# Kernel tuning notes

Measured on AMD Instinct MI355X. Metric: run time of the kernel, lower is better.

## Reference

```python
import jax, jax.numpy as jnp
import numpy as np

N = 50000
E = 800000
NEG_SLOPE = 0.2  # PyG GATConv default negative_slope


def _gat_layer(x, src, dst, W, a_src, a_dst, b, concat):
    # x: [N, Fin]; src/dst: [Etot] (self-loops already appended)
    H, O = a_src.shape
    n = x.shape[0]
    h = (x @ W).reshape(n, H, O)                      # [N, H, O]
    e_src = jnp.einsum('nho,ho->nh', h, a_src)        # [N, H]
    e_dst = jnp.einsum('nho,ho->nh', h, a_dst)
    alpha = e_src[src] + e_dst[dst]                   # [Etot, H]
    alpha = jnp.where(alpha >= 0, alpha, NEG_SLOPE * alpha)
    # segment softmax over destination nodes
    amax = jax.ops.segment_max(alpha, dst, num_segments=n)
    ex = jnp.exp(alpha - amax[dst])
    denom = jax.ops.segment_sum(ex, dst, num_segments=n)
    att = ex / (denom[dst] + 1e-16)                   # [Etot, H]
    msg = h[src] * att[:, :, None]                    # [Etot, H, O]
    agg = jax.ops.segment_sum(msg, dst, num_segments=n)  # [N, H, O]
    out = agg.reshape(n, H * O) if concat else agg.mean(axis=1)
    return out + b


def setup_inputs() -> dict:
    key = jax.random.key(0)
    k0, k1 = jax.random.split(key)
    inp = {
        'x': jax.random.normal(k0, (N, 2), jnp.float32),
        'edge_index': jax.random.randint(k1, (2, E), 0, N),
    }
    s = 0.1
    dims = [(2, 4, 64), (256, 4, 64), (256, 1, 2)]
    for i, (fin, H, O) in enumerate(dims):
        kw, ks, kd = jax.random.split(jax.random.fold_in(key, i + 10), 3)
        inp[f'W{i}'] = jax.random.normal(kw, (fin, H * O), jnp.float32) * s
        inp[f'a_src{i}'] = jax.random.normal(ks, (H, O), jnp.float32) * s
        inp[f'a_dst{i}'] = jax.random.normal(kd, (H, O), jnp.float32) * s
        inp[f'b{i}'] = jnp.zeros((H * O if i < 2 else O,), jnp.float32)
    return inp


def reference(x, edge_index, W0, a_src0, a_dst0, b0, W1, a_src1, a_dst1, b1,
              W2, a_src2, a_dst2, b2):
    n = x.shape[0]
    loops = jnp.arange(n, dtype=edge_index.dtype)  # PyG add_self_loops=True
    src = jnp.concatenate([edge_index[0], loops])
    dst = jnp.concatenate([edge_index[1], loops])
    h = jax.nn.relu(_gat_layer(x, src, dst, W0, a_src0, a_dst0, b0, True))
    h = jax.nn.relu(_gat_layer(h, src, dst, W1, a_src1, a_dst1, b1, True))
    h = jax.nn.relu(_gat_layer(h, src, dst, W2, a_src2, a_dst2, b2, False))
    return h
```

## Files before the change

kernel.cpp:

```cpp
#include <hip/hip_runtime.h>
#include <math.h>


typedef __attribute__((ext_vector_type(8))) short s16x8;
typedef __attribute__((ext_vector_type(4))) float f32x4;
typedef unsigned short u16;

__device__ __forceinline__ float wred_sum(float v){
  #pragma unroll
  for (int m = 32; m > 0; m >>= 1) v += __shfl_xor(v, m, 64);
  return v;
}
__device__ __forceinline__ void wred_sum4(float4& v){
  #pragma unroll
  for (int m = 32; m > 0; m >>= 1){
    v.x += __shfl_xor(v.x, m, 64);
    v.y += __shfl_xor(v.y, m, 64);
    v.z += __shfl_xor(v.z, m, 64);
    v.w += __shfl_xor(v.w, m, 64);
  }
}
__device__ __forceinline__ u16 bf16_rne(float x){
  unsigned int u = __float_as_uint(x);
  unsigned int r = u + 0x7FFFu + ((u >> 16) & 1u);
  return (u16)(r >> 16);
}

__global__ __launch_bounds__(256) void k_setup(const float* __restrict__ W1, u16* __restrict__ WhT,
                                               u16* __restrict__ WlT,
                                               const float* __restrict__ W0, const float* __restrict__ as0,
                                               const float* __restrict__ ad0, float* __restrict__ vs,
                                               int* __restrict__ deg, int N, int nblk_deg){
  int b = blockIdx.x;
  if (b < nblk_deg){
    int i = b * 256 + threadIdx.x;
    if (i < N) deg[i] = 1;
  } else if (b < nblk_deg + 256){
    int k = b - nblk_deg, j = threadIdx.x;
    float w = W1[k * 256 + j];
    u16 h = bf16_rne(w);
    float hf = __uint_as_float(((unsigned int)h) << 16);
    WhT[j * 256 + k] = h;
    WlT[j * 256 + k] = bf16_rne(w - hf);
  } else {
    int t = threadIdx.x;
    if (t < 8){
      int j = t >> 2, h = t & 3;
      float ss = 0.f, dd = 0.f;
      #pragma unroll 8
      for (int o = 0; o < 64; o++){
        float w = W0[j * 256 + h * 64 + o];
        ss = fmaf(w, as0[h * 64 + o], ss);
        dd = fmaf(w, ad0[h * 64 + o], dd);
      }
      vs[j * 4 + h]     = ss;
      vs[8 + j * 4 + h] = dd;
    }
  }
}

__global__ __launch_bounds__(256) void k_hist(const int* __restrict__ dst, int E, int* deg){
  int e = blockIdx.x * 256 + threadIdx.x;
  if (e < E) atomicAdd(&deg[dst[e]], 1);
}

__global__ __launch_bounds__(256) void k_scan_local(const int* __restrict__ deg, int* __restrict__ rowptr,
                                                    int* __restrict__ bsum, int N){
  __shared__ int sb[256];
  int t = threadIdx.x;
  int base = blockIdx.x * 2048 + t * 8;
  int d[8], s = 0;
  #pragma unroll
  for (int k = 0; k < 8; k++){
    d[k] = (base + k < N) ? deg[base + k] : 0;
    s += d[k];
  }
  sb[t] = s;
  __syncthreads();
  for (int off = 1; off < 256; off <<= 1){
    int v = (t >= off) ? sb[t - off] : 0;
    __syncthreads();
    sb[t] += v;
    __syncthreads();
  }
  int run = (t == 0) ? 0 : sb[t - 1];
  #pragma unroll
  for (int k = 0; k < 8; k++){
    if (base + k < N) rowptr[base + k] = run;
    run += d[k];
  }
  if (t == 255) bsum[blockIdx.x] = sb[255];
}

__global__ __launch_bounds__(256) void k_finish(int* __restrict__ rowptr, const int* __restrict__ bsum,
                                                int* __restrict__ ssrc, int* __restrict__ cursor,
                                                int N, int nb){
  __shared__ int off_sh;
  int i = blockIdx.x * 256 + threadIdx.x;
  if (threadIdx.x == 0){
    int bk = blockIdx.x >> 3;
    int s = 0;
    for (int k = 0; k < bk; k++) s += bsum[k];
    off_sh = s;
  }
  __syncthreads();
  if (i < N){
    int p = rowptr[i] + off_sh;
    rowptr[i] = p;
    ssrc[p] = i;
    cursor[i] = p + 1;
  }
  if (i == 0){
    int s = 0;
    for (int k = 0; k < nb; k++) s += bsum[k];
    rowptr[N] = s;
  }
}

__global__ __launch_bounds__(256) void k_scatter(const int* __restrict__ src, const int* __restrict__ dst,
                                                 int E, int* cursor, int* ssrc){
  int e = blockIdx.x * 256 + threadIdx.x;
  if (e < E){ int p = atomicAdd(&cursor[dst[e]], 1); ssrc[p] = src[e]; }
}

__global__ __launch_bounds__(256) void k_edge0(const float* __restrict__ X, const float* __restrict__ vs,
                                               const int* __restrict__ rowptr, const int* __restrict__ ssrc,
                                               float* __restrict__ agg2, int N){
  int lane = threadIdx.x & 63;
  int n = blockIdx.x * 4 + (threadIdx.x >> 6);
  if (n >= N) return;
  int start = rowptr[n], deg = rowptr[n + 1] - start;
  float4 va = ((const float4*)vs)[0], vb = ((const float4*)vs)[1];
  float4 vc = ((const float4*)vs)[2], vd = ((const float4*)vs)[3];
  float2 xn = ((const float2*)X)[n];
  float4 ed4;
  ed4.x = fmaf(xn.x, vc.x, xn.y * vd.x); ed4.y = fmaf(xn.x, vc.y, xn.y * vd.y);
  ed4.z = fmaf(xn.x, vc.z, xn.y * vd.z); ed4.w = fmaf(xn.x, vc.w, xn.y * vd.w);

  float4 den = make_float4(0.f,0.f,0.f,0.f);
  float4 a0  = make_float4(0.f,0.f,0.f,0.f);
  float4 a1  = make_float4(0.f,0.f,0.f,0.f);
  for (int i = lane; i < deg; i += 64){
    int s = ssrc[start + i];
    float2 xs = ((const float2*)X)[s];
    float4 e;
    e.x = fmaf(xs.x, va.x, fmaf(xs.y, vb.x, ed4.x));
    e.y = fmaf(xs.x, va.y, fmaf(xs.y, vb.y, ed4.y));
    e.z = fmaf(xs.x, va.z, fmaf(xs.y, vb.z, ed4.z));
    e.w = fmaf(xs.x, va.w, fmaf(xs.y, vb.w, ed4.w));
    e.x = fmaxf(e.x, 0.2f*e.x); e.y = fmaxf(e.y, 0.2f*e.y);
    e.z = fmaxf(e.z, 0.2f*e.z); e.w = fmaxf(e.w, 0.2f*e.w);
    float4 wt;
    wt.x = __expf(e.x); wt.y = __expf(e.y);
    wt.z = __expf(e.z); wt.w = __expf(e.w);
    den.x += wt.x; den.y += wt.y; den.z += wt.z; den.w += wt.w;
    a0.x = fmaf(wt.x, xs.x, a0.x); a0.y = fmaf(wt.y, xs.x, a0.y);
    a0.z = fmaf(wt.z, xs.x, a0.z); a0.w = fmaf(wt.w, xs.x, a0.w);
    a1.x = fmaf(wt.x, xs.y, a1.x); a1.y = fmaf(wt.y, xs.y, a1.y);
    a1.z = fmaf(wt.z, xs.y, a1.z); a1.w = fmaf(wt.w, xs.y, a1.w);
  }
  wred_sum4(den); wred_sum4(a0); wred_sum4(a1);

  if (lane == 0){
    float4 inv;
    inv.x = 1.f / (den.x + 1e-16f); inv.y = 1.f / (den.y + 1e-16f);
    inv.z = 1.f / (den.z + 1e-16f); inv.w = 1.f / (den.w + 1e-16f);
    float4 gA, gB;
    gA.x = a0.x * inv.x; gA.y = a1.x * inv.x;
    gA.z = a0.y * inv.y; gA.w = a1.y * inv.y;
    gB.x = a0.z * inv.z; gB.y = a1.z * inv.z;
    gB.z = a0.w * inv.w; gB.w = a1.w * inv.w;
    float4* g = (float4*)(agg2 + (size_t)n * 8);
    g[0] = gA; g[1] = gB;
  }
}

__global__ __launch_bounds__(256) void k_l1_mfma(const float* __restrict__ agg2,
                                                 const float* __restrict__ W0, const float* __restrict__ b0,
                                                 const u16* __restrict__ WhT, const u16* __restrict__ WlT,
                                                 const float* __restrict__ as_, const float* __restrict__ ad_,
                                                 u16* __restrict__ Hh16, float* __restrict__ ES,
                                                 float* __restrict__ ED, int N){
  __shared__ u16 Ah[64 * 32], Al[64 * 32];
  __shared__ u16 Bh[256 * 32], Bl[256 * 32];
  int t = threadIdx.x;
  int wv = t >> 6, lane = t & 63;
  int lr = lane & 15, lg = lane >> 4;
  int rb = blockIdx.x * 64;

  f32x4 acc[16];
  #pragma unroll
  for (int c = 0; c < 16; c++) acc[c] = (f32x4){0.f, 0.f, 0.f, 0.f};

  int arow = t >> 2, aseg = t & 3;
  int agrow = rb + arow;
  float4 ga = make_float4(0.f,0.f,0.f,0.f), gb = make_float4(0.f,0.f,0.f,0.f);
  if (agrow < N){
    const float4* g = (const float4*)(agg2 + (size_t)agrow * 8);
    ga = g[0]; gb = g[1];
  }

  for (int ks = 0; ks < 8; ks++){
    int k0 = ks * 32;
    __syncthreads();
    {
      int c0 = k0 + aseg * 8;
      int h = c0 >> 6;
      float g0 = (h==0)?ga.x:(h==1)?ga.z:(h==2)?gb.x:gb.z;
      float g1 = (h==0)?ga.y:(h==1)?ga.w:(h==2)?gb.y:gb.w;
      float4 w0a = *(const float4*)(W0 + c0);
      float4 w0b = *(const float4*)(W0 + c0 + 4);
      float4 w1a = *(const float4*)(W0 + 256 + c0);
      float4 w1b = *(const float4*)(W0 + 256 + c0 + 4);
      float4 bba = *(const float4*)(b0 + c0);
      float4 bbb = *(const float4*)(b0 + c0 + 4);
      float xv[8];
      xv[0] = fmaxf(fmaf(g0, w0a.x, fmaf(g1, w1a.x, bba.x)), 0.f);
      xv[1] = fmaxf(fmaf(g0, w0a.y, fmaf(g1, w1a.y, bba.y)), 0.f);
      xv[2] = fmaxf(fmaf(g0, w0a.z, fmaf(g1, w1a.z, bba.z)), 0.f);
      xv[3] = fmaxf(fmaf(g0, w0a.w, fmaf(g1, w1a.w, bba.w)), 0.f);
      xv[4] = fmaxf(fmaf(g0, w0b.x, fmaf(g1, w1b.x, bbb.x)), 0.f);
      xv[5] = fmaxf(fmaf(g0, w0b.y, fmaf(g1, w1b.y, bbb.y)), 0.f);
      xv[6] = fmaxf(fmaf(g0, w0b.z, fmaf(g1, w1b.z, bbb.z)), 0.f);
      xv[7] = fmaxf(fmaf(g0, w0b.w, fmaf(g1, w1b.w, bbb.w)), 0.f);
      if (agrow >= N){
        #pragma unroll
        for (int i = 0; i < 8; i++) xv[i] = 0.f;
      }
      union { u16 us[8]; uint4 v; } ph, pl;
      #pragma unroll
      for (int i = 0; i < 8; i++){
        u16 h16 = bf16_rne(xv[i]);
        float hf = __uint_as_float(((unsigned int)h16) << 16);
        ph.us[i] = h16;
        pl.us[i] = bf16_rne(xv[i] - hf);
      }
      *(uint4*)&Ah[arow * 32 + aseg * 8] = ph.v;
      *(uint4*)&Al[arow * 32 + aseg * 8] = pl.v;
    }
    #pragma unroll
    for (int i = 0; i < 4; i++){
      int chunk = i * 256 + t;
      int j = chunk >> 2, seg = chunk & 3;
      *(uint4*)&Bh[j * 32 + seg * 8] = *(const uint4*)&WhT[j * 256 + k0 + seg * 8];
      *(uint4*)&Bl[j * 32 + seg * 8] = *(const uint4*)&WlT[j * 256 + k0 + seg * 8];
    }
    __syncthreads();
    s16x8 ah = *(const s16x8*)&Ah[(wv * 16 + lr) * 32 + lg * 8];
    s16x8 al = *(const s16x8*)&Al[(wv * 16 + lr) * 32 + lg * 8];
    #pragma unroll
    for (int c = 0; c < 16; c++){
      s16x8 bh = *(const s16x8*)&Bh[(c * 16 + lr) * 32 + lg * 8];
      s16x8 bl = *(const s16x8*)&Bl[(c * 16 + lr) * 32 + lg * 8];
      acc[c] = __builtin_amdgcn_mfma_f32_16x16x32_bf16(ah, bh, acc[c], 0, 0, 0);
      acc[c] = __builtin_amdgcn_mfma_f32_16x16x32_bf16(ah, bl, acc[c], 0, 0, 0);
      acc[c] = __builtin_amdgcn_mfma_f32_16x16x32_bf16(al, bh, acc[c], 0, 0, 0);
    }
  }

  #pragma unroll
  for (int q = 0; q < 4; q++){
    int n = rb + wv * 16 + lg * 4 + q;
    if (n < N){
      union { _Float16 h[16]; uint4 v[2]; } pk;
      #pragma unroll
      for (int c = 0; c < 16; c++) pk.h[c] = (_Float16)acc[c][q];
      uint4* dstp = (uint4*)(Hh16 + (size_t)n * 256 + lr * 16);
      dstp[0] = pk.v[0];
      dstp[1] = pk.v[1];
    }
  }
  float es_p[4][4], ed_p[4][4];
  #pragma unroll
  for (int h = 0; h < 4; h++)
    #pragma unroll
    for (int q = 0; q < 4; q++){ es_p[h][q] = 0.f; ed_p[h][q] = 0.f; }
  #pragma unroll
  for (int c = 0; c < 16; c++){
    float asv = as_[c * 16 + lr];
    float adv = ad_[c * 16 + lr];
    int h = c >> 2;
    #pragma unroll
    for (int q = 0; q < 4; q++){
      es_p[h][q] = fmaf(acc[c][q], asv, es_p[h][q]);
      ed_p[h][q] = fmaf(acc[c][q], adv, ed_p[h][q]);
    }
  }
  #pragma unroll
  for (int h = 0; h < 4; h++)
    #pragma unroll
    for (int q = 0; q < 4; q++){
      #pragma unroll
      for (int mk = 1; mk < 16; mk <<= 1){
        es_p[h][q] += __shfl_xor(es_p[h][q], mk, 64);
        ed_p[h][q] += __shfl_xor(ed_p[h][q], mk, 64);
      }
    }
  if (lr == 0){
    #pragma unroll
    for (int q = 0; q < 4; q++){
      int n = rb + wv * 16 + lg * 4 + q;
      if (n < N){
        #pragma unroll
        for (int h = 0; h < 4; h++){
          ES[n * 4 + h] = es_p[h][q];
          ED[n * 4 + h] = ed_p[h][q];
        }
      }
    }
  }
}

__device__ __forceinline__ void agg_rows16(const u16* __restrict__ Hh, const int* ssh, const float* wrow,
                                           int cl, int lane, float* acc){
  union Cv { uint2 u; _Float16 h[4]; };
  int j = 0;
  for (; j + 7 < cl; j += 8){
    Cv r0, r1, r2, r3, r4, r5, r6, r7;
    float w0=wrow[j],w1=wrow[j+1],w2=wrow[j+2],w3=wrow[j+3];
    float w4=wrow[j+4],w5=wrow[j+5],w6=wrow[j+6],w7=wrow[j+7];
    r0.u = *(const uint2*)(Hh + (size_t)ssh[j  ] * 256 + 4*lane);
    r1.u = *(const uint2*)(Hh + (size_t)ssh[j+1] * 256 + 4*lane);
    r2.u = *(const uint2*)(Hh + (size_t)ssh[j+2] * 256 + 4*lane);
    r3.u = *(const uint2*)(Hh + (size_t)ssh[j+3] * 256 + 4*lane);
    r4.u = *(const uint2*)(Hh + (size_t)ssh[j+4] * 256 + 4*lane);
    r5.u = *(const uint2*)(Hh + (size_t)ssh[j+5] * 256 + 4*lane);
    r6.u = *(const uint2*)(Hh + (size_t)ssh[j+6] * 256 + 4*lane);
    r7.u = *(const uint2*)(Hh + (size_t)ssh[j+7] * 256 + 4*lane);
    #pragma unroll
    for (int k = 0; k < 4; k++) acc[k] = fmaf(w0, (float)r0.h[k], acc[k]);
    #pragma unroll
    for (int k = 0; k < 4; k++) acc[k] = fmaf(w1, (float)r1.h[k], acc[k]);
    #pragma unroll
    for (int k = 0; k < 4; k++) acc[k] = fmaf(w2, (float)r2.h[k], acc[k]);
    #pragma unroll
    for (int k = 0; k < 4; k++) acc[k] = fmaf(w3, (float)r3.h[k], acc[k]);
    #pragma unroll
    for (int k = 0; k < 4; k++) acc[k] = fmaf(w4, (float)r4.h[k], acc[k]);
    #pragma unroll
    for (int k = 0; k < 4; k++) acc[k] = fmaf(w5, (float)r5.h[k], acc[k]);
    #pragma unroll
    for (int k = 0; k < 4; k++) acc[k] = fmaf(w6, (float)r6.h[k], acc[k]);
    #pragma unroll
    for (int k = 0; k < 4; k++) acc[k] = fmaf(w7, (float)r7.h[k], acc[k]);
  }
  for (; j + 3 < cl; j += 4){
    Cv r0, r1, r2, r3;
    float w0=wrow[j],w1=wrow[j+1],w2=wrow[j+2],w3=wrow[j+3];
    r0.u = *(const uint2*)(Hh + (size_t)ssh[j  ] * 256 + 4*lane);
    r1.u = *(const uint2*)(Hh + (size_t)ssh[j+1] * 256 + 4*lane);
    r2.u = *(const uint2*)(Hh + (size_t)ssh[j+2] * 256 + 4*lane);
    r3.u = *(const uint2*)(Hh + (size_t)ssh[j+3] * 256 + 4*lane);
    #pragma unroll
    for (int k = 0; k < 4; k++) acc[k] = fmaf(w0, (float)r0.h[k], acc[k]);
    #pragma unroll
    for (int k = 0; k < 4; k++) acc[k] = fmaf(w1, (float)r1.h[k], acc[k]);
    #pragma unroll
    for (int k = 0; k < 4; k++) acc[k] = fmaf(w2, (float)r2.h[k], acc[k]);
    #pragma unroll
    for (int k = 0; k < 4; k++) acc[k] = fmaf(w3, (float)r3.h[k], acc[k]);
  }
  for (; j < cl; ++j){
    Cv r0;
    float w0 = wrow[j];
    r0.u = *(const uint2*)(Hh + (size_t)ssh[j] * 256 + 4*lane);
    #pragma unroll
    for (int k = 0; k < 4; k++) acc[k] = fmaf(w0, (float)r0.h[k], acc[k]);
  }
}

__global__ __launch_bounds__(64) void k_edge1(const u16* __restrict__ Hh16, const float* __restrict__ ES,
                                              const float* __restrict__ ED, const int* __restrict__ rowptr,
                                              const int* __restrict__ ssrc, const float* __restrict__ b1,
                                              const float* __restrict__ W2,
                                              const float* __restrict__ as2, const float* __restrict__ ad2,
                                              float* __restrict__ P2, int N){
  __shared__ int   ssh[64];
  __shared__ float wsh[4][68];
  int lane = threadIdx.x;
  int n = blockIdx.x;
  int myhead = lane & 3;
  int start = rowptr[n], deg = rowptr[n + 1] - start;
  float4 ed4 = ((const float4*)ED)[n];

  float accv[4] = {0.f, 0.f, 0.f, 0.f};
  float4 den = make_float4(0.f,0.f,0.f,0.f);

  for (int base = 0; base < deg; base += 64){
    int i = base + lane;
    float4 wt = make_float4(0.f,0.f,0.f,0.f);
    int s = 0;
    if (i < deg){
      s = ssrc[start + i];
      float4 e = ((const float4*)ES)[s];
      e.x += ed4.x; e.y += ed4.y; e.z += ed4.z; e.w += ed4.w;
      e.x = fmaxf(e.x, 0.2f*e.x); e.y = fmaxf(e.y, 0.2f*e.y);
      e.z = fmaxf(e.z, 0.2f*e.z); e.w = fmaxf(e.w, 0.2f*e.w);
      wt.x = __expf(e.x); wt.y = __expf(e.y);
      wt.z = __expf(e.z); wt.w = __expf(e.w);
    }
    den.x += wt.x; den.y += wt.y; den.z += wt.z; den.w += wt.w;
    ssh[lane] = s;
    wsh[0][lane] = wt.x; wsh[1][lane] = wt.y;
    wsh[2][lane] = wt.z; wsh[3][lane] = wt.w;
    __syncthreads();
    agg_rows16(Hh16, ssh, wsh[myhead], min(deg - base, 64), lane, accv);
    __syncthreads();
  }

  wred_sum4(den);
  float d = (myhead==0)?den.x:(myhead==1)?den.y:(myhead==2)?den.z:den.w;
  float inv = 1.f / (d + 1e-16f);
  int c0 = 64 * (lane & 3) + (lane >> 2);
  float p0 = 0.f, p1 = 0.f;
  #pragma unroll
  for (int j = 0; j < 4; j++){
    int col = c0 + 16 * j;
    float v = fmaxf(fmaf(accv[j], inv, b1[col]), 0.f);
    float2 w2 = ((const float2*)W2)[col];
    p0 = fmaf(v, w2.x, p0);
    p1 = fmaf(v, w2.y, p1);
  }
  p0 = wred_sum(p0); p1 = wred_sum(p1);
  if (lane == 0){
    float4 o;
    o.x = p0; o.y = p1;
    o.z = p0*as2[0] + p1*as2[1];
    o.w = p0*ad2[0] + p1*ad2[1];
    ((float4*)P2)[n] = o;
  }
}

__global__ __launch_bounds__(256) void k_edge2(const float* __restrict__ P2, const int* __restrict__ rowptr,
                                               const int* __restrict__ ssrc, const float* __restrict__ bias,
                                               float* __restrict__ Out, int N){
  int lane = threadIdx.x & 63;
  int n = blockIdx.x * 4 + (threadIdx.x >> 6);
  if (n >= N) return;
  int start = rowptr[n], deg = rowptr[n + 1] - start;
  float edn = ((const float4*)P2)[n].w;
  float den = 0.f, a0 = 0.f, a1 = 0.f;
  for (int i = lane; i < deg; i += 64){
    int s = ssrc[start + i];
    float4 p = ((const float4*)P2)[s];
    float a = p.z + edn; a = fmaxf(a, 0.2f * a);
    float w = __expf(a);
    den += w;
    a0 = fmaf(w, p.x, a0);
    a1 = fmaf(w, p.y, a1);
  }
  den = wred_sum(den); a0 = wred_sum(a0); a1 = wred_sum(a1);
  if (lane == 0){
    float inv = 1.f / (den + 1e-16f);
    Out[n*2]     = fmaxf(a0 * inv + bias[0], 0.f);
    Out[n*2 + 1] = fmaxf(a1 * inv + bias[1], 0.f);
  }
}

extern "C" void kernel_launch(void* const* d_in, const int* in_sizes, int n_in,
                              void* d_out, int out_size, void* d_ws, size_t ws_size,
                              hipStream_t stream) {
  const float* x   = (const float*)d_in[0];
  const int*   ei  = (const int*)  d_in[1];
  const float* W0  = (const float*)d_in[2];
  const float* as0 = (const float*)d_in[3];
  const float* ad0 = (const float*)d_in[4];
  const float* b0  = (const float*)d_in[5];
  const float* W1  = (const float*)d_in[6];
  const float* as1 = (const float*)d_in[7];
  const float* ad1 = (const float*)d_in[8];
  const float* b1  = (const float*)d_in[9];
  const float* W2  = (const float*)d_in[10];
  const float* as2 = (const float*)d_in[11];
  const float* ad2 = (const float*)d_in[12];
  const float* b2  = (const float*)d_in[13];

  int N = in_sizes[0] / 2;
  int E = in_sizes[1] / 2;
  const int* src = ei;
  const int* dst = ei + E;

  char* ws = (char*)d_ws;
  size_t off = 0;
  auto alc = [&](size_t bytes){ size_t o = off; off += (bytes + 255) & ~(size_t)255; return o; };
  int*   deg    = (int*)(ws + alc((size_t)N * 4));
  int*   rowptr = (int*)(ws + alc((size_t)(N + 1) * 4));
  int*   cursor = (int*)(ws + alc((size_t)N * 4));
  int*   ssrc   = (int*)(ws + alc((size_t)(E + N) * 4));
  u16*   Hh16   = (u16*)  (ws + alc((size_t)N * 256 * 2));
  float* agg2   = (float*)(ws + alc((size_t)N * 8 * 4));
  float* es1    = (float*)(ws + alc((size_t)N * 4 * 4));
  float* ed1    = (float*)(ws + alc((size_t)N * 4 * 4));
  float* P2     = (float*)(ws + alc((size_t)N * 4 * 4));
  u16*   wht    = (u16*)  (ws + alc((size_t)256 * 256 * 2));
  u16*   wlt    = (u16*)  (ws + alc((size_t)256 * 256 * 2));
  float* vs     = (float*)(ws + alc(16 * 4));
  int*   bsum   = (int*)(ws + alc(64 * 4));
  float* out    = (float*)d_out;

  int nblk_deg = (N + 255) / 256;
  int nb = (N + 2047) / 2048;

  k_setup     <<<nblk_deg + 257, 256, 0, stream>>>(W1, wht, wlt, W0, as0, ad0, vs, deg, N, nblk_deg);
  k_hist      <<<(E + 255)/256, 256, 0, stream>>>(dst, E, deg);
  k_scan_local<<<nb, 256, 0, stream>>>(deg, rowptr, bsum, N);
  k_finish    <<<nblk_deg, 256, 0, stream>>>(rowptr, bsum, ssrc, cursor, N, nb);
  k_scatter   <<<(E + 255)/256, 256, 0, stream>>>(src, dst, E, cursor, ssrc);

  k_edge0  <<<(N + 3)/4, 256, 0, stream>>>(x, vs, rowptr, ssrc, agg2, N);
  k_l1_mfma<<<(N + 63)/64, 256, 0, stream>>>(agg2, W0, b0, wht, wlt, as1, ad1, Hh16, es1, ed1, N);
  k_edge1  <<<N, 64, 0, stream>>>(Hh16, es1, ed1, rowptr, ssrc, b1, W2, as2, ad2, P2, N);
  k_edge2  <<<(N + 3)/4, 256, 0, stream>>>(P2, rowptr, ssrc, b2, out, N);
}
```

Before: 345.0 us.

## Fuse layer-0 edge aggregation into layer-1 MFMA kernel and merge histogram into setup

Computes the layer-0 attention aggregation inside the layer-1 GEMM kernel, now 512 threads with 128 rows per block, and hands results to the A-tile producers through a lane-select. This removes the agg2 round trip and one launch. The degree histogram moves into the setup kernel, with deg zeroed by a memset and the self-loop +1 added in the scan, which drops another launch. In exchange, each wave serially processes 16 nodes before any MFMA work starts, and the larger block may lower occupancy.

```diff
diff --git a/kernel.cpp b/kernel.cpp
--- a/kernel.cpp
+++ b/kernel.cpp
@@ -26,17 +26,18 @@
   return (u16)(r >> 16);
 }
 
-__global__ __launch_bounds__(256) void k_setup(const float* __restrict__ W1, u16* __restrict__ WhT,
-                                               u16* __restrict__ WlT,
-                                               const float* __restrict__ W0, const float* __restrict__ as0,
-                                               const float* __restrict__ ad0, float* __restrict__ vs,
-                                               int* __restrict__ deg, int N, int nblk_deg){
+__global__ __launch_bounds__(256) void k_prep(const int* __restrict__ dst, int E, int* __restrict__ deg,
+                                              const float* __restrict__ W1, u16* __restrict__ WhT,
+                                              u16* __restrict__ WlT,
+                                              const float* __restrict__ W0, const float* __restrict__ as0,
+                                              const float* __restrict__ ad0, float* __restrict__ vs,
+                                              int nhist){
   int b = blockIdx.x;
-  if (b < nblk_deg){
-    int i = b * 256 + threadIdx.x;
-    if (i < N) deg[i] = 1;
-  } else if (b < nblk_deg + 256){
-    int k = b - nblk_deg, j = threadIdx.x;
+  if (b < nhist){
+    int e = b * 256 + threadIdx.x;
+    if (e < E) atomicAdd(&deg[dst[e]], 1);
+  } else if (b < nhist + 256){
+    int k = b - nhist, j = threadIdx.x;
     float w = W1[k * 256 + j];
     u16 h = bf16_rne(w);
     float hf = __uint_as_float(((unsigned int)h) << 16);
@@ -59,11 +60,6 @@
   }
 }
 
-__global__ __launch_bounds__(256) void k_hist(const int* __restrict__ dst, int E, int* deg){
-  int e = blockIdx.x * 256 + threadIdx.x;
-  if (e < E) atomicAdd(&deg[dst[e]], 1);
-}
-
 __global__ __launch_bounds__(256) void k_scan_local(const int* __restrict__ deg, int* __restrict__ rowptr,
                                                     int* __restrict__ bsum, int N){
   __shared__ int sb[256];
@@ -72,7 +68,7 @@
   int d[8], s = 0;
   #pragma unroll
   for (int k = 0; k < 8; k++){
-    d[k] = (base + k < N) ? deg[base + k] : 0;
+    d[k] = (base + k < N) ? (deg[base + k] + 1) : 0;
     s += d[k];
   }
   sb[t] = s;
@@ -123,45 +119,54 @@
   if (e < E){ int p = atomicAdd(&cursor[dst[e]], 1); ssrc[p] = src[e]; }
 }
 
-__global__ __launch_bounds__(256) void k_edge0(const float* __restrict__ X, const float* __restrict__ vs,
-                                               const int* __restrict__ rowptr, const int* __restrict__ ssrc,
-                                               float* __restrict__ agg2, int N){
-  int lane = threadIdx.x & 63;
-  int n = blockIdx.x * 4 + (threadIdx.x >> 6);
-  if (n >= N) return;
-  int start = rowptr[n], deg = rowptr[n + 1] - start;
+__global__ __launch_bounds__(512) void k_l1f(const float* __restrict__ X, const float* __restrict__ vs,
+                                             const int* __restrict__ rowptr, const int* __restrict__ ssrc,
+                                             const float* __restrict__ W0, const float* __restrict__ b0,
+                                             const u16* __restrict__ WhT, const u16* __restrict__ WlT,
+                                             const float* __restrict__ as_, const float* __restrict__ ad_,
+                                             u16* __restrict__ Hh16, float* __restrict__ ES,
+                                             float* __restrict__ ED, int N){
+  __shared__ u16 Ah[128 * 32], Al[128 * 32];
+  __shared__ u16 Bh[256 * 32], Bl[256 * 32];
+  int t = threadIdx.x;
+  int wv = t >> 6, lane = t & 63;
+  int lr = lane & 15, lg = lane >> 4;
+  int rb = blockIdx.x * 128;
+
   float4 va = ((const float4*)vs)[0], vb = ((const float4*)vs)[1];
   float4 vc = ((const float4*)vs)[2], vd = ((const float4*)vs)[3];
-  float2 xn = ((const float2*)X)[n];
-  float4 ed4;
-  ed4.x = fmaf(xn.x, vc.x, xn.y * vd.x); ed4.y = fmaf(xn.x, vc.y, xn.y * vd.y);
-  ed4.z = fmaf(xn.x, vc.z, xn.y * vd.z); ed4.w = fmaf(xn.x, vc.w, xn.y * vd.w);
-
-  float4 den = make_float4(0.f,0.f,0.f,0.f);
-  float4 a0  = make_float4(0.f,0.f,0.f,0.f);
-  float4 a1  = make_float4(0.f,0.f,0.f,0.f);
-  for (int i = lane; i < deg; i += 64){
-    int s = ssrc[start + i];
-    float2 xs = ((const float2*)X)[s];
-    float4 e;
-    e.x = fmaf(xs.x, va.x, fmaf(xs.y, vb.x, ed4.x));
-    e.y = fmaf(xs.x, va.y, fmaf(xs.y, vb.y, ed4.y));
-    e.z = fmaf(xs.x, va.z, fmaf(xs.y, vb.z, ed4.z));
-    e.w = fmaf(xs.x, va.w, fmaf(xs.y, vb.w, ed4.w));
-    e.x = fmaxf(e.x, 0.2f*e.x); e.y = fmaxf(e.y, 0.2f*e.y);
-    e.z = fmaxf(e.z, 0.2f*e.z); e.w = fmaxf(e.w, 0.2f*e.w);
-    float4 wt;
-    wt.x = __expf(e.x); wt.y = __expf(e.y);
-    wt.z = __expf(e.z); wt.w = __expf(e.w);
-    den.x += wt.x; den.y += wt.y; den.z += wt.z; den.w += wt.w;
-    a0.x = fmaf(wt.x, xs.x, a0.x); a0.y = fmaf(wt.y, xs.x, a0.y);
-    a0.z = fmaf(wt.z, xs.x, a0.z); a0.w = fmaf(wt.w, xs.x, a0.w);
-    a1.x = fmaf(wt.x, xs.y, a1.x); a1.y = fmaf(wt.y, xs.y, a1.y);
-    a1.z = fmaf(wt.z, xs.y, a1.z); a1.w = fmaf(wt.w, xs.y, a1.w);
-  }
-  wred_sum4(den); wred_sum4(a0); wred_sum4(a1);
-
-  if (lane == 0){
+  float4 myga = make_float4(0.f,0.f,0.f,0.f), mygb = make_float4(0.f,0.f,0.f,0.f);
+  for (int i = 0; i < 16; i++){
+    int n = rb + wv * 16 + i;
+    if (n >= N) break;
+    int start = rowptr[n], deg = rowptr[n + 1] - start;
+    float2 xn = ((const float2*)X)[n];
+    float4 ed4;
+    ed4.x = fmaf(xn.x, vc.x, xn.y * vd.x); ed4.y = fmaf(xn.x, vc.y, xn.y * vd.y);
+    ed4.z = fmaf(xn.x, vc.z, xn.y * vd.z); ed4.w = fmaf(xn.x, vc.w, xn.y * vd.w);
+    float4 den = make_float4(0.f,0.f,0.f,0.f);
+    float4 a0  = make_float4(0.f,0.f,0.f,0.f);
+    float4 a1  = make_float4(0.f,0.f,0.f,0.f);
+    for (int idx = lane; idx < deg; idx += 64){
+      int s = ssrc[start + idx];
+      float2 xs = ((const float2*)X)[s];
+      float4 e;
+      e.x = fmaf(xs.x, va.x, fmaf(xs.y, vb.x, ed4.x));
+      e.y = fmaf(xs.x, va.y, fmaf(xs.y, vb.y, ed4.y));
+      e.z = fmaf(xs.x, va.z, fmaf(xs.y, vb.z, ed4.z));
+      e.w = fmaf(xs.x, va.w, fmaf(xs.y, vb.w, ed4.w));
+      e.x = fmaxf(e.x, 0.2f*e.x); e.y = fmaxf(e.y, 0.2f*e.y);
+      e.z = fmaxf(e.z, 0.2f*e.z); e.w = fmaxf(e.w, 0.2f*e.w);
+      float4 wt;
+      wt.x = __expf(e.x); wt.y = __expf(e.y);
+      wt.z = __expf(e.z); wt.w = __expf(e.w);
+      den.x += wt.x; den.y += wt.y; den.z += wt.z; den.w += wt.w;
+      a0.x = fmaf(wt.x, xs.x, a0.x); a0.y = fmaf(wt.y, xs.x, a0.y);
+      a0.z = fmaf(wt.z, xs.x, a0.z); a0.w = fmaf(wt.w, xs.x, a0.w);
+      a1.x = fmaf(wt.x, xs.y, a1.x); a1.y = fmaf(wt.y, xs.y, a1.y);
+      a1.z = fmaf(wt.z, xs.y, a1.z); a1.w = fmaf(wt.w, xs.y, a1.w);
+    }
+    wred_sum4(den); wred_sum4(a0); wred_sum4(a1);
     float4 inv;
     inv.x = 1.f / (den.x + 1e-16f); inv.y = 1.f / (den.y + 1e-16f);
     inv.z = 1.f / (den.z + 1e-16f); inv.w = 1.f / (den.w + 1e-16f);
@@ -170,23 +175,8 @@
     gA.z = a0.y * inv.y; gA.w = a1.y * inv.y;
     gB.x = a0.z * inv.z; gB.y = a1.z * inv.z;
     gB.z = a0.w * inv.w; gB.w = a1.w * inv.w;
-    float4* g = (float4*)(agg2 + (size_t)n * 8);
-    g[0] = gA; g[1] = gB;
-  }
-}
-
-__global__ __launch_bounds__(256) void k_l1_mfma(const float* __restrict__ agg2,
-                                                 const float* __restrict__ W0, const float* __restrict__ b0,
-                                                 const u16* __restrict__ WhT, const u16* __restrict__ WlT,
-                                                 const float* __restrict__ as_, const float* __restrict__ ad_,
-                                                 u16* __restrict__ Hh16, float* __restrict__ ES,
-                                                 float* __restrict__ ED, int N){
-  __shared__ u16 Ah[64 * 32], Al[64 * 32];
-  __shared__ u16 Bh[256 * 32], Bl[256 * 32];
-  int t = threadIdx.x;
-  int wv = t >> 6, lane = t & 63;
-  int lr = lane & 15, lg = lane >> 4;
-  int rb = blockIdx.x * 64;
+    if ((lane >> 2) == i){ myga = gA; mygb = gB; }
+  }
 
   f32x4 acc[16];
   #pragma unroll
@@ -194,11 +184,6 @@
 
   int arow = t >> 2, aseg = t & 3;
   int agrow = rb + arow;
-  float4 ga = make_float4(0.f,0.f,0.f,0.f), gb = make_float4(0.f,0.f,0.f,0.f);
-  if (agrow < N){
-    const float4* g = (const float4*)(agg2 + (size_t)agrow * 8);
-    ga = g[0]; gb = g[1];
-  }
 
   for (int ks = 0; ks < 8; ks++){
     int k0 = ks * 32;
@@ -206,8 +191,8 @@
     {
       int c0 = k0 + aseg * 8;
       int h = c0 >> 6;
-      float g0 = (h==0)?ga.x:(h==1)?ga.z:(h==2)?gb.x:gb.z;
-      float g1 = (h==0)?ga.y:(h==1)?ga.w:(h==2)?gb.y:gb.w;
+      float g0 = (h==0)?myga.x:(h==1)?myga.z:(h==2)?mygb.x:mygb.z;
+      float g1 = (h==0)?myga.y:(h==1)?myga.w:(h==2)?mygb.y:mygb.w;
       float4 w0a = *(const float4*)(W0 + c0);
       float4 w0b = *(const float4*)(W0 + c0 + 4);
       float4 w1a = *(const float4*)(W0 + 256 + c0);
@@ -239,8 +224,8 @@
       *(uint4*)&Al[arow * 32 + aseg * 8] = pl.v;
     }
     #pragma unroll
-    for (int i = 0; i < 4; i++){
-      int chunk = i * 256 + t;
+    for (int i = 0; i < 2; i++){
+      int chunk = i * 512 + t;
       int j = chunk >> 2, seg = chunk & 3;
       *(uint4*)&Bh[j * 32 + seg * 8] = *(const uint4*)&WhT[j * 256 + k0 + seg * 8];
       *(uint4*)&Bl[j * 32 + seg * 8] = *(const uint4*)&WlT[j * 256 + k0 + seg * 8];
@@ -488,7 +473,6 @@
   int*   cursor = (int*)(ws + alc((size_t)N * 4));
   int*   ssrc   = (int*)(ws + alc((size_t)(E + N) * 4));
   u16*   Hh16   = (u16*)  (ws + alc((size_t)N * 256 * 2));
-  float* agg2   = (float*)(ws + alc((size_t)N * 8 * 4));
   float* es1    = (float*)(ws + alc((size_t)N * 4 * 4));
   float* ed1    = (float*)(ws + alc((size_t)N * 4 * 4));
   float* P2     = (float*)(ws + alc((size_t)N * 4 * 4));
@@ -498,17 +482,18 @@
   int*   bsum   = (int*)(ws + alc(64 * 4));
   float* out    = (float*)d_out;
 
-  int nblk_deg = (N + 255) / 256;
-  int nb = (N + 2047) / 2048;
-
-  k_setup     <<<nblk_deg + 257, 256, 0, stream>>>(W1, wht, wlt, W0, as0, ad0, vs, deg, N, nblk_deg);
-  k_hist      <<<(E + 255)/256, 256, 0, stream>>>(dst, E, deg);
+  int nhist  = (E + 255) / 256;
+  int nblk_n = (N + 255) / 256;
+  int nb     = (N + 2047) / 2048;
+
+  hipMemsetAsync(deg, 0, (size_t)N * 4, stream);
+  k_prep      <<<nhist + 257, 256, 0, stream>>>(dst, E, deg, W1, wht, wlt, W0, as0, ad0, vs, nhist);
   k_scan_local<<<nb, 256, 0, stream>>>(deg, rowptr, bsum, N);
-  k_finish    <<<nblk_deg, 256, 0, stream>>>(rowptr, bsum, ssrc, cursor, N, nb);
-  k_scatter   <<<(E + 255)/256, 256, 0, stream>>>(src, dst, E, cursor, ssrc);
-
-  k_edge0  <<<(N + 3)/4, 256, 0, stream>>>(x, vs, rowptr, ssrc, agg2, N);
-  k_l1_mfma<<<(N + 63)/64, 256, 0, stream>>>(agg2, W0, b0, wht, wlt, as1, ad1, Hh16, es1, ed1, N);
-  k_edge1  <<<N, 64, 0, stream>>>(Hh16, es1, ed1, rowptr, ssrc, b1, W2, as2, ad2, P2, N);
-  k_edge2  <<<(N + 3)/4, 256, 0, stream>>>(P2, rowptr, ssrc, b2, out, N);
-}
+  k_finish    <<<nblk_n, 256, 0, stream>>>(rowptr, bsum, ssrc, cursor, N, nb);
+  k_scatter   <<<nhist, 256, 0, stream>>>(src, dst, E, cursor, ssrc);
+
+  k_l1f  <<<(N + 127)/128, 512, 0, stream>>>(x, vs, rowptr, ssrc, W0, b0, wht, wlt,
+                                             as1, ad1, Hh16, es1, ed1, N);
+  k_edge1<<<N, 64, 0, stream>>>(Hh16, es1, ed1, rowptr, ssrc, b1, W2, as2, ad2, P2, N);
+  k_edge2<<<(N + 3)/4, 256, 0, stream>>>(P2, rowptr, ssrc, b2, out, N);
+}
```

New measurement: 350.1 us. Within noise of the previous version (+1.5%).

## Widen edge1 gathers to 16-byte loads across half-waves; merge histogram into prep

Applied to the files above, without the earlier changes.

In the layer-2 aggregation kernel, each lane now loads 8 fp16 values (16 bytes) per neighbor row. The two half-waves take alternating edges, and their partial sums are combined with a cross-half shuffle before the epilogue. This halves the number of gather instructions and issues wider memory transactions per neighbor. The degree histogram is folded into the setup kernel, which removes one launch. The degree init is replaced by a memset, with the self-loop +1 moved into the scan. The epilogue column mapping and per-head normalization are rewritten to match the new accumulator layout, which risks indexing mistakes.

```diff
diff --git a/kernel.cpp b/kernel.cpp
--- a/kernel.cpp
+++ b/kernel.cpp
@@ -26,17 +26,18 @@
   return (u16)(r >> 16);
 }
 
-__global__ __launch_bounds__(256) void k_setup(const float* __restrict__ W1, u16* __restrict__ WhT,
-                                               u16* __restrict__ WlT,
-                                               const float* __restrict__ W0, const float* __restrict__ as0,
-                                               const float* __restrict__ ad0, float* __restrict__ vs,
-                                               int* __restrict__ deg, int N, int nblk_deg){
+__global__ __launch_bounds__(256) void k_prep(const int* __restrict__ dst, int E, int* __restrict__ deg,
+                                              const float* __restrict__ W1, u16* __restrict__ WhT,
+                                              u16* __restrict__ WlT,
+                                              const float* __restrict__ W0, const float* __restrict__ as0,
+                                              const float* __restrict__ ad0, float* __restrict__ vs,
+                                              int nhist){
   int b = blockIdx.x;
-  if (b < nblk_deg){
-    int i = b * 256 + threadIdx.x;
-    if (i < N) deg[i] = 1;
-  } else if (b < nblk_deg + 256){
-    int k = b - nblk_deg, j = threadIdx.x;
+  if (b < nhist){
+    int e = b * 256 + threadIdx.x;
+    if (e < E) atomicAdd(&deg[dst[e]], 1);
+  } else if (b < nhist + 256){
+    int k = b - nhist, j = threadIdx.x;
     float w = W1[k * 256 + j];
     u16 h = bf16_rne(w);
     float hf = __uint_as_float(((unsigned int)h) << 16);
@@ -59,11 +60,6 @@
   }
 }
 
-__global__ __launch_bounds__(256) void k_hist(const int* __restrict__ dst, int E, int* deg){
-  int e = blockIdx.x * 256 + threadIdx.x;
-  if (e < E) atomicAdd(&deg[dst[e]], 1);
-}
-
 __global__ __launch_bounds__(256) void k_scan_local(const int* __restrict__ deg, int* __restrict__ rowptr,
                                                     int* __restrict__ bsum, int N){
   __shared__ int sb[256];
@@ -72,7 +68,7 @@
   int d[8], s = 0;
   #pragma unroll
   for (int k = 0; k < 8; k++){
-    d[k] = (base + k < N) ? deg[base + k] : 0;
+    d[k] = (base + k < N) ? (deg[base + k] + 1) : 0;
     s += d[k];
   }
   sb[t] = s;
@@ -311,64 +307,6 @@
   }
 }
 
-__device__ __forceinline__ void agg_rows16(const u16* __restrict__ Hh, const int* ssh, const float* wrow,
-                                           int cl, int lane, float* acc){
-  union Cv { uint2 u; _Float16 h[4]; };
-  int j = 0;
-  for (; j + 7 < cl; j += 8){
-    Cv r0, r1, r2, r3, r4, r5, r6, r7;
-    float w0=wrow[j],w1=wrow[j+1],w2=wrow[j+2],w3=wrow[j+3];
-    float w4=wrow[j+4],w5=wrow[j+5],w6=wrow[j+6],w7=wrow[j+7];
-    r0.u = *(const uint2*)(Hh + (size_t)ssh[j  ] * 256 + 4*lane);
-    r1.u = *(const uint2*)(Hh + (size_t)ssh[j+1] * 256 + 4*lane);
-    r2.u = *(const uint2*)(Hh + (size_t)ssh[j+2] * 256 + 4*lane);
-    r3.u = *(const uint2*)(Hh + (size_t)ssh[j+3] * 256 + 4*lane);
-    r4.u = *(const uint2*)(Hh + (size_t)ssh[j+4] * 256 + 4*lane);
-    r5.u = *(const uint2*)(Hh + (size_t)ssh[j+5] * 256 + 4*lane);
-    r6.u = *(const uint2*)(Hh + (size_t)ssh[j+6] * 256 + 4*lane);
-    r7.u = *(const uint2*)(Hh + (size_t)ssh[j+7] * 256 + 4*lane);
-    #pragma unroll
-    for (int k = 0; k < 4; k++) acc[k] = fmaf(w0, (float)r0.h[k], acc[k]);
-    #pragma unroll
-    for (int k = 0; k < 4; k++) acc[k] = fmaf(w1, (float)r1.h[k], acc[k]);
-    #pragma unroll
-    for (int k = 0; k < 4; k++) acc[k] = fmaf(w2, (float)r2.h[k], acc[k]);
-    #pragma unroll
-    for (int k = 0; k < 4; k++) acc[k] = fmaf(w3, (float)r3.h[k], acc[k]);
-    #pragma unroll
-    for (int k = 0; k < 4; k++) acc[k] = fmaf(w4, (float)r4.h[k], acc[k]);
-    #pragma unroll
-    for (int k = 0; k < 4; k++) acc[k] = fmaf(w5, (float)r5.h[k], acc[k]);
-    #pragma unroll
-    for (int k = 0; k < 4; k++) acc[k] = fmaf(w6, (float)r6.h[k], acc[k]);
-    #pragma unroll
-    for (int k = 0; k < 4; k++) acc[k] = fmaf(w7, (float)r7.h[k], acc[k]);
-  }
-  for (; j + 3 < cl; j += 4){
-    Cv r0, r1, r2, r3;
-    float w0=wrow[j],w1=wrow[j+1],w2=wrow[j+2],w3=wrow[j+3];
-    r0.u = *(const uint2*)(Hh + (size_t)ssh[j  ] * 256 + 4*lane);
-    r1.u = *(const uint2*)(Hh + (size_t)ssh[j+1] * 256 + 4*lane);
-    r2.u = *(const uint2*)(Hh + (size_t)ssh[j+2] * 256 + 4*lane);
-    r3.u = *(const uint2*)(Hh + (size_t)ssh[j+3] * 256 + 4*lane);
-    #pragma unroll
-    for (int k = 0; k < 4; k++) acc[k] = fmaf(w0, (float)r0.h[k], acc[k]);
-    #pragma unroll
-    for (int k = 0; k < 4; k++) acc[k] = fmaf(w1, (float)r1.h[k], acc[k]);
-    #pragma unroll
-    for (int k = 0; k < 4; k++) acc[k] = fmaf(w2, (float)r2.h[k], acc[k]);
-    #pragma unroll
-    for (int k = 0; k < 4; k++) acc[k] = fmaf(w3, (float)r3.h[k], acc[k]);
-  }
-  for (; j < cl; ++j){
-    Cv r0;
-    float w0 = wrow[j];
-    r0.u = *(const uint2*)(Hh + (size_t)ssh[j] * 256 + 4*lane);
-    #pragma unroll
-    for (int k = 0; k < 4; k++) acc[k] = fmaf(w0, (float)r0.h[k], acc[k]);
-  }
-}
-
 __global__ __launch_bounds__(64) void k_edge1(const u16* __restrict__ Hh16, const float* __restrict__ ES,
                                               const float* __restrict__ ED, const int* __restrict__ rowptr,
                                               const int* __restrict__ ssrc, const float* __restrict__ b1,
@@ -379,12 +317,18 @@
   __shared__ float wsh[4][68];
   int lane = threadIdx.x;
   int n = blockIdx.x;
-  int myhead = lane & 3;
   int start = rowptr[n], deg = rowptr[n + 1] - start;
   float4 ed4 = ((const float4*)ED)[n];
 
-  float accv[4] = {0.f, 0.f, 0.f, 0.f};
+  int half = lane >> 5;
+  int l32  = lane & 31;
+  int hA = 2 * (l32 & 1);
+  int hB = hA + 1;
+  const u16* rowbase = Hh16 + 8 * l32;
+
+  float acc8[8] = {0.f,0.f,0.f,0.f,0.f,0.f,0.f,0.f};
   float4 den = make_float4(0.f,0.f,0.f,0.f);
+  union Cv { uint4 v; _Float16 h[8]; };
 
   for (int base = 0; base < deg; base += 64){
     int i = base + lane;
@@ -404,22 +348,90 @@
     wsh[0][lane] = wt.x; wsh[1][lane] = wt.y;
     wsh[2][lane] = wt.z; wsh[3][lane] = wt.w;
     __syncthreads();
-    agg_rows16(Hh16, ssh, wsh[myhead], min(deg - base, 64), lane, accv);
+    int cl = min(deg - base, 64);
+    const float* wrA = wsh[hA];
+    const float* wrB = wsh[hB];
+    int j = half;
+    for (; j + 14 < cl; j += 16){
+      int s0=ssh[j],s1=ssh[j+2],s2=ssh[j+4],s3=ssh[j+6];
+      int s4=ssh[j+8],s5=ssh[j+10],s6=ssh[j+12],s7=ssh[j+14];
+      float wa0=wrA[j],wb0=wrB[j],wa1=wrA[j+2],wb1=wrB[j+2];
+      float wa2=wrA[j+4],wb2=wrB[j+4],wa3=wrA[j+6],wb3=wrB[j+6];
+      float wa4=wrA[j+8],wb4=wrB[j+8],wa5=wrA[j+10],wb5=wrB[j+10];
+      float wa6=wrA[j+12],wb6=wrB[j+12],wa7=wrA[j+14],wb7=wrB[j+14];
+      Cv r0,r1,r2,r3,r4,r5,r6,r7;
+      r0.v = *(const uint4*)(rowbase + (size_t)s0*256);
+      r1.v = *(const uint4*)(rowbase + (size_t)s1*256);
+      r2.v = *(const uint4*)(rowbase + (size_t)s2*256);
+      r3.v = *(const uint4*)(rowbase + (size_t)s3*256);
+      r4.v = *(const uint4*)(rowbase + (size_t)s4*256);
+      r5.v = *(const uint4*)(rowbase + (size_t)s5*256);
+      r6.v = *(const uint4*)(rowbase + (size_t)s6*256);
+      r7.v = *(const uint4*)(rowbase + (size_t)s7*256);
+      #pragma unroll
+      for (int k = 0; k < 4; k++) acc8[k] = fmaf(wa0, (float)r0.h[k], acc8[k]);
+      #pragma unroll
+      for (int k = 4; k < 8; k++) acc8[k] = fmaf(wb0, (float)r0.h[k], acc8[k]);
+      #pragma unroll
+      for (int k = 0; k < 4; k++) acc8[k] = fmaf(wa1, (float)r1.h[k], acc8[k]);
+      #pragma unroll
+      for (int k = 4; k < 8; k++) acc8[k] = fmaf(wb1, (float)r1.h[k], acc8[k]);
+      #pragma unroll
+      for (int k = 0; k < 4; k++) acc8[k] = fmaf(wa2, (float)r2.h[k], acc8[k]);
+      #pragma unroll
+      for (int k = 4; k < 8; k++) acc8[k] = fmaf(wb2, (float)r2.h[k], acc8[k]);
+      #pragma unroll
+      for (int k = 0; k < 4; k++) acc8[k] = fmaf(wa3, (float)r3.h[k], acc8[k]);
+      #pragma unroll
+      for (int k = 4; k < 8; k++) acc8[k] = fmaf(wb3, (float)r3.h[k], acc8[k]);
+      #pragma unroll
+      for (int k = 0; k < 4; k++) acc8[k] = fmaf(wa4, (float)r4.h[k], acc8[k]);
+      #pragma unroll
+      for (int k = 4; k < 8; k++) acc8[k] = fmaf(wb4, (float)r4.h[k], acc8[k]);
+      #pragma unroll
+      for (int k = 0; k < 4; k++) acc8[k] = fmaf(wa5, (float)r5.h[k], acc8[k]);
+      #pragma unroll
+      for (int k = 4; k < 8; k++) acc8[k] = fmaf(wb5, (float)r5.h[k], acc8[k]);
+      #pragma unroll
+      for (int k = 0; k < 4; k++) acc8[k] = fmaf(wa6, (float)r6.h[k], acc8[k]);
+      #pragma unroll
+      for (int k = 4; k < 8; k++) acc8[k] = fmaf(wb6, (float)r6.h[k], acc8[k]);
+      #pragma unroll
+      for (int k = 0; k < 4; k++) acc8[k] = fmaf(wa7, (float)r7.h[k], acc8[k]);
+      #pragma unroll
+      for (int k = 4; k < 8; k++) acc8[k] = fmaf(wb7, (float)r7.h[k], acc8[k]);
+    }
+    for (; j < cl; j += 2){
+      int s0 = ssh[j];
+      float wa = wrA[j], wb = wrB[j];
+      Cv r;
+      r.v = *(const uint4*)(rowbase + (size_t)s0*256);
+      #pragma unroll
+      for (int k = 0; k < 4; k++) acc8[k] = fmaf(wa, (float)r.h[k], acc8[k]);
+      #pragma unroll
+      for (int k = 4; k < 8; k++) acc8[k] = fmaf(wb, (float)r.h[k], acc8[k]);
+    }
     __syncthreads();
   }
 
+  #pragma unroll
+  for (int k = 0; k < 8; k++) acc8[k] += __shfl_xor(acc8[k], 32, 64);
   wred_sum4(den);
-  float d = (myhead==0)?den.x:(myhead==1)?den.y:(myhead==2)?den.z:den.w;
-  float inv = 1.f / (d + 1e-16f);
-  int c0 = 64 * (lane & 3) + (lane >> 2);
+  float invA = 1.f / (((hA == 0) ? den.x : den.z) + 1e-16f);
+  float invB = 1.f / (((hB == 1) ? den.y : den.w) + 1e-16f);
+
   float p0 = 0.f, p1 = 0.f;
-  #pragma unroll
-  for (int j = 0; j < 4; j++){
-    int col = c0 + 16 * j;
-    float v = fmaxf(fmaf(accv[j], inv, b1[col]), 0.f);
-    float2 w2 = ((const float2*)W2)[col];
-    p0 = fmaf(v, w2.x, p0);
-    p1 = fmaf(v, w2.y, p1);
+  if (half == 0){
+    #pragma unroll
+    for (int k = 0; k < 8; k++){
+      int p = 8 * l32 + k;
+      int col = (p & 15) * 16 + (p >> 4);
+      float inv = (k < 4) ? invA : invB;
+      float v = fmaxf(fmaf(acc8[k], inv, b1[col]), 0.f);
+      float2 w2 = ((const float2*)W2)[col];
+      p0 = fmaf(v, w2.x, p0);
+      p1 = fmaf(v, w2.y, p1);
+    }
   }
   p0 = wred_sum(p0); p1 = wred_sum(p1);
   if (lane == 0){
@@ -498,14 +510,15 @@
   int*   bsum   = (int*)(ws + alc(64 * 4));
   float* out    = (float*)d_out;
 
-  int nblk_deg = (N + 255) / 256;
-  int nb = (N + 2047) / 2048;
-
-  k_setup     <<<nblk_deg + 257, 256, 0, stream>>>(W1, wht, wlt, W0, as0, ad0, vs, deg, N, nblk_deg);
-  k_hist      <<<(E + 255)/256, 256, 0, stream>>>(dst, E, deg);
+  int nhist  = (E + 255) / 256;
+  int nblk_n = (N + 255) / 256;
+  int nb     = (N + 2047) / 2048;
+
+  hipMemsetAsync(deg, 0, (size_t)N * 4, stream);
+  k_prep      <<<nhist + 257, 256, 0, stream>>>(dst, E, deg, W1, wht, wlt, W0, as0, ad0, vs, nhist);
   k_scan_local<<<nb, 256, 0, stream>>>(deg, rowptr, bsum, N);
-  k_finish    <<<nblk_deg, 256, 0, stream>>>(rowptr, bsum, ssrc, cursor, N, nb);
-  k_scatter   <<<(E + 255)/256, 256, 0, stream>>>(src, dst, E, cursor, ssrc);
+  k_finish    <<<nblk_n, 256, 0, stream>>>(rowptr, bsum, ssrc, cursor, N, nb);
+  k_scatter   <<<nhist, 256, 0, stream>>>(src, dst, E, cursor, ssrc);
 
   k_edge0  <<<(N + 3)/4, 256, 0, stream>>>(x, vs, rowptr, ssrc, agg2, N);
   k_l1_mfma<<<(N + 63)/64, 256, 0, stream>>>(agg2, W0, b0, wht, wlt, as1, ad1, Hh16, es1, ed1, N);
```

Measured after the change: 337.8 us. -2.1%, faster.
